# Kernel optimization log

Hardware: AMD Instinct MI355X
Metric: run time of the kernel (lower is better)

Reference implementation:

```python
import jax, jax.numpy as jnp
import numpy as np

N_NODES = 50000
N_EDGES = 800000
NEG_SLOPE = 0.2  # PyG GATConv default


def _glorot(key, shape):
    fan_in = shape[0] if len(shape) > 1 else shape[0]
    return jax.random.normal(key, shape, dtype=jnp.float32) / jnp.sqrt(jnp.float32(fan_in))


def setup_inputs() -> dict:
    key = jax.random.key(0)
    ks = jax.random.split(key, 12)
    x = jax.random.normal(ks[0], (N_NODES, 128), dtype=jnp.float32)
    edge_index = jax.random.randint(ks[1], (2, N_EDGES), 0, N_NODES, dtype=jnp.int64)
    return {
        "x": x,
        "edge_index": edge_index,
        # GAT layer 1: 128 -> 128 (heads=1)
        "W1": _glorot(ks[2], (128, 128)),
        "a_src1": _glorot(ks[3], (128,)),
        "a_dst1": _glorot(ks[4], (128,)),
        "b1": jnp.zeros((128,), dtype=jnp.float32),
        "Wres1": _glorot(ks[5], (128, 128)),
        # GAT layer 2: 128 -> 256
        "W2": _glorot(ks[6], (128, 256)),
        "a_src2": _glorot(ks[7], (256,)),
        "a_dst2": _glorot(ks[8], (256,)),
        "b2": jnp.zeros((256,), dtype=jnp.float32),
        "Wres2": _glorot(ks[9], (128, 256)),
    }


def _gat_layer(x, src, dst, W, a_src, a_dst, b, Wres, n):
    # h: [N, C_out] transformed node features
    h = x @ W
    # per-edge attention logit: gather scalar contributions, LeakyReLU
    logit = jax.nn.leaky_relu((h @ a_src)[src] + (h @ a_dst)[dst], NEG_SLOPE)  # [E]
    # numerically stable segment softmax over incoming edges of each dst node
    seg_max = jax.ops.segment_max(logit, dst, num_segments=n)  # [N]
    ex = jnp.exp(logit - seg_max[dst])
    denom = jax.ops.segment_sum(ex, dst, num_segments=n)  # [N]
    alpha = ex / denom[dst]  # [E]; self-loops guarantee denom > 0
    # weighted scatter-add aggregation
    out = jax.ops.segment_sum(alpha[:, None] * h[src], dst, num_segments=n)  # [N, C_out]
    # residual projection (in_dim != out_dim) + bias
    return out + x @ Wres + b


def reference(x, edge_index, W1, a_src1, a_dst1, b1, Wres1, W2, a_src2, a_dst2, b2, Wres2):
    n = x.shape[0]
    loops = jnp.arange(n, dtype=edge_index.dtype)  # add_self_loops=True (PyG default)
    src = jnp.concatenate([edge_index[0], loops])
    dst = jnp.concatenate([edge_index[1], loops])
    h = _gat_layer(x, src, dst, W1, a_src1, a_dst1, b1, Wres1, n)
    h = jax.nn.relu(h)
    return _gat_layer(h, src, dst, W2, a_src2, a_dst2, b2, Wres2, n)
```

## Files before the change

### kernel.cpp

```cpp
#include <hip/hip_runtime.h>
#include <math.h>

typedef __attribute__((ext_vector_type(8))) short bf16x8;
typedef __attribute__((ext_vector_type(4))) float f32x4;

__device__ inline unsigned short f2bf(float f) {
  union { float f; unsigned u; } x; x.f = f;
  unsigned r = x.u + 0x7FFF + ((x.u >> 16) & 1);
  return (unsigned short)(r >> 16);
}
__device__ inline float bf2f(unsigned short b) {
  union { unsigned u; float f; } x; x.u = ((unsigned)b) << 16;
  return x.f;
}


__global__ void convert_kernel(const void* edges, int E, int N,
                               int* __restrict__ src32, int* __restrict__ dst32,
                               int* __restrict__ counts) {
  int i = blockIdx.x * blockDim.x + threadIdx.x;
  int tot = E + N;
  if (i >= tot) return;
  int s, d;
  if (i < E) {
    const long long* q = (const long long*)edges;
    bool i64 = true;
#pragma unroll
    for (int k = 0; k < 8; ++k) {
      long long v = q[k];
      if (v < 0 || v >= (long long)N) i64 = false;
    }
    if (i64) {
      s = (int)q[i];
      d = (int)q[E + i];
    } else {
      s = ((const int*)edges)[i];
      d = ((const int*)edges)[E + i];
    }
  } else {
    s = d = i - E;
  }
  src32[i] = s;
  dst32[i] = d;
  atomicAdd(&counts[d], 1);
}


__global__ __launch_bounds__(256) void scan_partial(const int* __restrict__ counts,
                                                    int* __restrict__ bsum, int n) {
  int t = threadIdx.x;
  int base = blockIdx.x * 1024 + t * 4;
  int s = 0;
#pragma unroll
  for (int k = 0; k < 4; ++k) {
    int i = base + k;
    if (i < n) s += counts[i];
  }
#pragma unroll
  for (int off = 32; off; off >>= 1) s += __shfl_xor(s, off);
  __shared__ int red[4];
  if ((t & 63) == 0) red[t >> 6] = s;
  __syncthreads();
  if (t == 0) bsum[blockIdx.x] = red[0] + red[1] + red[2] + red[3];
}

__global__ __launch_bounds__(256) void scan_bsum(const int* __restrict__ bsum,
                                                 int* __restrict__ ebsum,
                                                 int* __restrict__ rowptr, int nblk, int n) {
  __shared__ int sh[256];
  int t = threadIdx.x;
  int v = (t < nblk) ? bsum[t] : 0;
  sh[t] = v;
  __syncthreads();
  for (int off = 1; off < 256; off <<= 1) {
    int u = (t >= off) ? sh[t - off] : 0;
    __syncthreads();
    sh[t] += u;
    __syncthreads();
  }
  if (t < nblk) ebsum[t] = sh[t] - v;
  if (t == nblk - 1) rowptr[n] = sh[t];
}

__global__ __launch_bounds__(256) void scan_final(const int* __restrict__ counts,
                                                  const int* __restrict__ ebsum,
                                                  int* __restrict__ rowptr,
                                                  int* __restrict__ cursor, int n) {
  int t = threadIdx.x;
  int lane = t & 63;
  int wv = t >> 6;
  int base = blockIdx.x * 1024 + t * 4;
  int c[4];
  int ts = 0;
#pragma unroll
  for (int k = 0; k < 4; ++k) {
    int i = base + k;
    c[k] = (i < n) ? counts[i] : 0;
    ts += c[k];
  }
  int ws = ts;
  for (int off = 1; off < 64; off <<= 1) {
    int u = __shfl_up(ws, off);
    if (lane >= off) ws += u;
  }
  __shared__ int wtot[4];
  if (lane == 63) wtot[wv] = ws;
  __syncthreads();
  int woff = 0;
  for (int k = 0; k < 4; ++k)
    if (k < wv) woff += wtot[k];
  int run = ebsum[blockIdx.x] + woff + (ws - ts);
#pragma unroll
  for (int k = 0; k < 4; ++k) {
    int i = base + k;
    if (i < n) {
      rowptr[i] = run;
      cursor[i] = run;
    }
    run += c[k];
  }
}

__global__ void scatter_kernel(const int* __restrict__ src32, const int* __restrict__ dst32,
                               int* __restrict__ cursor, int* __restrict__ csr_src, int tot) {
  int i = blockIdx.x * blockDim.x + threadIdx.x;
  if (i >= tot) return;
  int d = dst32[i];
  int slot = atomicAdd(&cursor[d], 1);
  csr_src[slot] = src32[i];
}


__global__ void cvt_x_kernel(const float* __restrict__ x, unsigned short* __restrict__ x16,
                             int N, int Mpad) {
  int tid = blockIdx.x * blockDim.x + threadIdx.x;
  if (tid >= Mpad * 32) return;
  int row = tid >> 5;
  int q = (tid & 31) << 2;
  unsigned short o0 = 0, o1 = 0, o2 = 0, o3 = 0;
  if (row < N) {
    float4 v = *(const float4*)(x + (size_t)row * 128 + q);
    o0 = f2bf(v.x); o1 = f2bf(v.y); o2 = f2bf(v.z); o3 = f2bf(v.w);
  }
  unsigned short* p = x16 + (size_t)row * 128 + q;
  p[0] = o0; p[1] = o1; p[2] = o2; p[3] = o3;
}

__global__ void cvt_wt_all(const float* __restrict__ W1, const float* __restrict__ Wres1,
                           const float* __restrict__ W2, const float* __restrict__ Wres2,
                           unsigned short* __restrict__ w1t, unsigned short* __restrict__ wres1t,
                           unsigned short* __restrict__ w2t, unsigned short* __restrict__ wres2t) {
  int tid = blockIdx.x * blockDim.x + threadIdx.x;
  const float* W;
  unsigned short* Wt;
  int C, loc;
  if (tid < 16384) { W = W1; Wt = w1t; C = 128; loc = tid; }
  else if (tid < 32768) { W = Wres1; Wt = wres1t; C = 128; loc = tid - 16384; }
  else if (tid < 65536) { W = W2; Wt = w2t; C = 256; loc = tid - 32768; }
  else if (tid < 98304) { W = Wres2; Wt = wres2t; C = 256; loc = tid - 65536; }
  else return;
  int c = loc >> 7;
  int k = loc & 127;
  Wt[(size_t)c * 128 + k] = f2bf(W[(size_t)k * C + c]);
}


template <int MODE>
__global__ __launch_bounds__(256) void gemm_mfma(const unsigned short* __restrict__ A,
                                                 const unsigned short* __restrict__ Bt,
                                                 void* __restrict__ Cout,
                                                 const float* __restrict__ bias,
                                                 int Nrows, int Ctot) {
  int l = threadIdx.x & 63;
  int w = threadIdx.x >> 6;
  int row_w = blockIdx.x * 128 + (w & 1) * 64;
  int col_w = blockIdx.y * 128 + (w >> 1) * 64;
  int lo = l & 15, hi = l >> 4;
  f32x4 acc[4][4];
#pragma unroll
  for (int i = 0; i < 4; ++i)
#pragma unroll
    for (int j = 0; j < 4; ++j) acc[i][j] = (f32x4){0.f, 0.f, 0.f, 0.f};

  const unsigned short* Ap = A + (size_t)(row_w + lo) * 128 + hi * 8;
  const unsigned short* Bp = Bt + (size_t)(col_w + lo) * 128 + hi * 8;
#pragma unroll
  for (int kk = 0; kk < 4; ++kk) {
    bf16x8 a[4], b[4];
#pragma unroll
    for (int f = 0; f < 4; ++f) {
      a[f] = *(const bf16x8*)(Ap + (size_t)f * 16 * 128 + kk * 32);
      b[f] = *(const bf16x8*)(Bp + (size_t)f * 16 * 128 + kk * 32);
    }
#pragma unroll
    for (int fr = 0; fr < 4; ++fr)
#pragma unroll
      for (int fc = 0; fc < 4; ++fc)
        acc[fr][fc] = __builtin_amdgcn_mfma_f32_16x16x32_bf16(a[fr], b[fc], acc[fr][fc], 0, 0, 0);
  }
#pragma unroll
  for (int fr = 0; fr < 4; ++fr) {
#pragma unroll
    for (int r = 0; r < 4; ++r) {
      int row = row_w + fr * 16 + hi * 4 + r;
      if (row < Nrows) {
#pragma unroll
        for (int fc = 0; fc < 4; ++fc) {
          int col = col_w + fc * 16 + lo;
          float v = acc[fr][fc][r];
          if (MODE != 0) v += bias[col];
          if (MODE == 2)
            ((float*)Cout)[(size_t)row * Ctot + col] = v;
          else
            ((unsigned short*)Cout)[(size_t)row * Ctot + col] = f2bf(v);
        }
      }
    }
  }
}


template <int C>
__global__ void scalars_kernel(const unsigned short* __restrict__ h,
                               const float* __restrict__ a_src,
                               const float* __restrict__ a_dst, float* __restrict__ as_,
                               float* __restrict__ ad_, int N) {
  int wid = (blockIdx.x * blockDim.x + threadIdx.x) >> 6;
  int lane = threadIdx.x & 63;
  if (wid >= N) return;
  const int FPL = C / 64;
  const unsigned short* hr = h + (size_t)wid * C + FPL * lane;
  float s1 = 0.f, s2 = 0.f;
#pragma unroll
  for (int j = 0; j < FPL; ++j) {
    float v = bf2f(hr[j]);
    s1 += v * a_src[FPL * lane + j];
    s2 += v * a_dst[FPL * lane + j];
  }
#pragma unroll
  for (int off = 32; off; off >>= 1) {
    s1 += __shfl_xor(s1, off);
    s2 += __shfl_xor(s2, off);
  }
  if (lane == 0) {
    as_[wid] = s1;
    ad_[wid] = s2;
  }
}


template <int C, bool BF16IO>
__global__ __launch_bounds__(256) void aggregate_kernel(
    const unsigned short* __restrict__ h, void* __restrict__ io,
    const float* __restrict__ as_, const float* __restrict__ ad_,
    const int* __restrict__ rowptr, const int* __restrict__ csr_src, int N) {
  const int FPL = C / 64;
  int wid = blockIdx.x * 4 + (threadIdx.x >> 6);
  int lane = threadIdx.x & 63;
  if (wid >= N) return;
  int base = rowptr[wid];
  int deg = rowptr[wid + 1] - base;
  float adn = ad_[wid];
  float m = -1e30f, ssum = 0.f;
  float acc[FPL];
#pragma unroll
  for (int c = 0; c < FPL; ++c) acc[c] = 0.f;
  for (int b0 = 0; b0 < deg; b0 += 64) {
    int idx = b0 + lane;
    int s = 0;
    float logit = -1e30f;
    if (idx < deg) {
      s = csr_src[base + idx];
      float tt = as_[s] + adn;
      logit = tt > 0.f ? tt : 0.2f * tt;
    }
    float cm = logit;
#pragma unroll
    for (int off = 32; off; off >>= 1) cm = fmaxf(cm, __shfl_xor(cm, off));
    float mnew = fmaxf(m, cm);
    float scale = __expf(m - mnew);
    ssum *= scale;
#pragma unroll
    for (int c = 0; c < FPL; ++c) acc[c] *= scale;
    float p = (idx < deg) ? __expf(logit - mnew) : 0.f;
    float ps = p;
#pragma unroll
    for (int off = 32; off; off >>= 1) ps += __shfl_xor(ps, off);
    ssum += ps;
    int cnt = min(64, deg - b0);
    for (int j = 0; j < cnt; ++j) {
      float pj = __shfl(p, j);
      int sj = __shfl(s, j);
      const unsigned short* hs = h + (size_t)sj * C + FPL * lane;
      if (FPL == 2) {
        ushort2 hv = *(const ushort2*)hs;
        acc[0] = fmaf(pj, bf2f(hv.x), acc[0]);
        acc[1] = fmaf(pj, bf2f(hv.y), acc[1]);
      } else {
        ushort4 hv = *(const ushort4*)hs;
        acc[0] = fmaf(pj, bf2f(hv.x), acc[0]);
        acc[1] = fmaf(pj, bf2f(hv.y), acc[1]);
        acc[2] = fmaf(pj, bf2f(hv.z), acc[2]);
        acc[3] = fmaf(pj, bf2f(hv.w), acc[3]);
      }
    }
    m = mnew;
  }
  float inv = 1.f / ssum;
  size_t o = (size_t)wid * C + FPL * lane;
  if (BF16IO) {
    unsigned short* p = (unsigned short*)io + o;
    ushort2 rv = *(const ushort2*)p;
    float v0 = fmaxf(acc[0] * inv + bf2f(rv.x), 0.f);
    float v1 = fmaxf(acc[1] * inv + bf2f(rv.y), 0.f);
    ushort2 ov; ov.x = f2bf(v0); ov.y = f2bf(v1);
    *(ushort2*)p = ov;
  } else {
    float* p = (float*)io + o;
    float4 rv = *(const float4*)p;
    float4 ov;
    ov.x = acc[0] * inv + rv.x;
    ov.y = acc[1] * inv + rv.y;
    ov.z = acc[2] * inv + rv.z;
    ov.w = acc[3] * inv + rv.w;
    *(float4*)p = ov;
  }
}


extern "C" void kernel_launch(void* const* d_in, const int* in_sizes, int n_in,
                              void* d_out, int out_size, void* d_ws, size_t ws_size,
                              hipStream_t stream) {
  const float* x = (const float*)d_in[0];
  const void* edges = d_in[1];
  const float* W1 = (const float*)d_in[2];
  const float* a_src1 = (const float*)d_in[3];
  const float* a_dst1 = (const float*)d_in[4];
  const float* b1 = (const float*)d_in[5];
  const float* Wres1 = (const float*)d_in[6];
  const float* W2 = (const float*)d_in[7];
  const float* a_src2 = (const float*)d_in[8];
  const float* a_dst2 = (const float*)d_in[9];
  const float* b2 = (const float*)d_in[10];
  const float* Wres2 = (const float*)d_in[11];
  float* out = (float*)d_out;

  int N = in_sizes[0] / 128;
  int E = in_sizes[1] / 2;
  int TOT = E + N;
  int Mpad = (N + 127) & ~127;
  int nblk = (N + 1023) >> 10;

  char* w = (char*)d_ws;
  size_t off = 0;
  auto alloc = [&](size_t bytes) {
    char* p = w + off;
    off += (bytes + 255) & ~(size_t)255;
    return p;
  };
  int* counts = (int*)alloc((size_t)N * 4);
  int* cursor = (int*)alloc((size_t)N * 4);
  int* rowptr = (int*)alloc((size_t)(N + 1) * 4);
  int* bsum = (int*)alloc(1024);
  int* ebsum = (int*)alloc(1024);
  float* as_ = (float*)alloc((size_t)N * 4);
  float* ad_ = (float*)alloc((size_t)N * 4);
  int* src32 = (int*)alloc((size_t)TOT * 4);
  int* dst32 = (int*)alloc((size_t)TOT * 4);
  int* csr = (int*)alloc((size_t)TOT * 4);
  unsigned short* x16 = (unsigned short*)alloc((size_t)Mpad * 128 * 2);
  unsigned short* w1t = (unsigned short*)alloc(128 * 128 * 2);
  unsigned short* wres1t = (unsigned short*)alloc(128 * 128 * 2);
  unsigned short* w2t = (unsigned short*)alloc(256 * 128 * 2);
  unsigned short* wres2t = (unsigned short*)alloc(256 * 128 * 2);
  unsigned short* h16 = (unsigned short*)alloc((size_t)N * 256 * 2);
  unsigned short* out1 = (unsigned short*)alloc((size_t)Mpad * 128 * 2);

  hipMemsetAsync(counts, 0, (size_t)N * 4, stream);
  hipMemsetAsync(out1 + (size_t)N * 128, 0, (size_t)(Mpad - N) * 128 * 2, stream);

  int gb = (TOT + 255) / 256;
  convert_kernel<<<gb, 256, 0, stream>>>(edges, E, N, src32, dst32, counts);
  scan_partial<<<nblk, 256, 0, stream>>>(counts, bsum, N);
  scan_bsum<<<1, 256, 0, stream>>>(bsum, ebsum, rowptr, nblk, N);
  scan_final<<<nblk, 256, 0, stream>>>(counts, ebsum, rowptr, cursor, N);
  scatter_kernel<<<gb, 256, 0, stream>>>(src32, dst32, cursor, csr, TOT);

  cvt_x_kernel<<<(Mpad * 32 + 255) / 256, 256, 0, stream>>>(x, x16, N, Mpad);
  cvt_wt_all<<<(98304 + 255) / 256, 256, 0, stream>>>(W1, Wres1, W2, Wres2, w1t, wres1t, w2t, wres2t);

  int mt = Mpad / 128;
  int sb = (N + 3) / 4;

  gemm_mfma<0><<<dim3(mt, 1), 256, 0, stream>>>(x16, w1t, h16, nullptr, N, 128);
  gemm_mfma<1><<<dim3(mt, 1), 256, 0, stream>>>(x16, wres1t, out1, b1, N, 128);
  scalars_kernel<128><<<sb, 256, 0, stream>>>(h16, a_src1, a_dst1, as_, ad_, N);
  aggregate_kernel<128, true><<<sb, 256, 0, stream>>>(h16, out1, as_, ad_, rowptr, csr, N);

  gemm_mfma<0><<<dim3(mt, 2), 256, 0, stream>>>(out1, w2t, h16, nullptr, N, 256);
  gemm_mfma<2><<<dim3(mt, 2), 256, 0, stream>>>(out1, wres2t, out, b2, N, 256);
  scalars_kernel<256><<<sb, 256, 0, stream>>>(h16, a_src2, a_dst2, as_, ad_, N);
  aggregate_kernel<256, false><<<sb, 256, 0, stream>>>(h16, out, as_, ad_, rowptr, csr, N);
}
```

Before: 429.8 us.

## Unroll aggregation gather by 4, store residual2 in bf16, merge conversion kernels

The edge-aggregation inner loop is unrolled four ways so four neighbour-row gathers are in flight at once, hiding more memory latency. The layer-2 residual projection now goes to a bf16 scratch buffer instead of read-modify-write on the fp32 output, which halves residual traffic. The x and weight conversion kernels are merged into one launch. The bf16 residual adds some rounding error to the final output.

```diff
diff --git a/kernel.cpp b/kernel.cpp
--- a/kernel.cpp
+++ b/kernel.cpp
@@ -131,33 +131,35 @@
 }
 
 
-__global__ void cvt_x_kernel(const float* __restrict__ x, unsigned short* __restrict__ x16,
-                             int N, int Mpad) {
+__global__ void cvt_all(const float* __restrict__ x,
+                        const float* __restrict__ W1, const float* __restrict__ Wres1,
+                        const float* __restrict__ W2, const float* __restrict__ Wres2,
+                        unsigned short* __restrict__ x16,
+                        unsigned short* __restrict__ w1t, unsigned short* __restrict__ wres1t,
+                        unsigned short* __restrict__ w2t, unsigned short* __restrict__ wres2t,
+                        int N, int Mpad) {
   int tid = blockIdx.x * blockDim.x + threadIdx.x;
-  if (tid >= Mpad * 32) return;
-  int row = tid >> 5;
-  int q = (tid & 31) << 2;
-  unsigned short o0 = 0, o1 = 0, o2 = 0, o3 = 0;
-  if (row < N) {
-    float4 v = *(const float4*)(x + (size_t)row * 128 + q);
-    o0 = f2bf(v.x); o1 = f2bf(v.y); o2 = f2bf(v.z); o3 = f2bf(v.w);
-  }
-  unsigned short* p = x16 + (size_t)row * 128 + q;
-  p[0] = o0; p[1] = o1; p[2] = o2; p[3] = o3;
-}
-
-__global__ void cvt_wt_all(const float* __restrict__ W1, const float* __restrict__ Wres1,
-                           const float* __restrict__ W2, const float* __restrict__ Wres2,
-                           unsigned short* __restrict__ w1t, unsigned short* __restrict__ wres1t,
-                           unsigned short* __restrict__ w2t, unsigned short* __restrict__ wres2t) {
-  int tid = blockIdx.x * blockDim.x + threadIdx.x;
+  int xcnt = Mpad * 32;
+  if (tid < xcnt) {
+    int row = tid >> 5;
+    int q = (tid & 31) << 2;
+    unsigned short o0 = 0, o1 = 0, o2 = 0, o3 = 0;
+    if (row < N) {
+      float4 v = *(const float4*)(x + (size_t)row * 128 + q);
+      o0 = f2bf(v.x); o1 = f2bf(v.y); o2 = f2bf(v.z); o3 = f2bf(v.w);
+    }
+    unsigned short* p = x16 + (size_t)row * 128 + q;
+    p[0] = o0; p[1] = o1; p[2] = o2; p[3] = o3;
+    return;
+  }
+  int t2 = tid - xcnt;
   const float* W;
   unsigned short* Wt;
   int C, loc;
-  if (tid < 16384) { W = W1; Wt = w1t; C = 128; loc = tid; }
-  else if (tid < 32768) { W = Wres1; Wt = wres1t; C = 128; loc = tid - 16384; }
-  else if (tid < 65536) { W = W2; Wt = w2t; C = 256; loc = tid - 32768; }
-  else if (tid < 98304) { W = Wres2; Wt = wres2t; C = 256; loc = tid - 65536; }
+  if (t2 < 16384) { W = W1; Wt = w1t; C = 128; loc = t2; }
+  else if (t2 < 32768) { W = Wres1; Wt = wres1t; C = 128; loc = t2 - 16384; }
+  else if (t2 < 65536) { W = W2; Wt = w2t; C = 256; loc = t2 - 32768; }
+  else if (t2 < 98304) { W = Wres2; Wt = wres2t; C = 256; loc = t2 - 65536; }
   else return;
   int c = loc >> 7;
   int k = loc & 127;
@@ -168,7 +170,7 @@
 template <int MODE>
 __global__ __launch_bounds__(256) void gemm_mfma(const unsigned short* __restrict__ A,
                                                  const unsigned short* __restrict__ Bt,
-                                                 void* __restrict__ Cout,
+                                                 unsigned short* __restrict__ Cout,
                                                  const float* __restrict__ bias,
                                                  int Nrows, int Ctot) {
   int l = threadIdx.x & 63;
@@ -208,11 +210,8 @@
         for (int fc = 0; fc < 4; ++fc) {
           int col = col_w + fc * 16 + lo;
           float v = acc[fr][fc][r];
-          if (MODE != 0) v += bias[col];
-          if (MODE == 2)
-            ((float*)Cout)[(size_t)row * Ctot + col] = v;
-          else
-            ((unsigned short*)Cout)[(size_t)row * Ctot + col] = f2bf(v);
+          if (MODE == 1) v += bias[col];
+          Cout[(size_t)row * Ctot + col] = f2bf(v);
         }
       }
     }
@@ -249,9 +248,10 @@
 }
 
 
-template <int C, bool BF16IO>
+template <int C, bool L1>
 __global__ __launch_bounds__(256) void aggregate_kernel(
-    const unsigned short* __restrict__ h, void* __restrict__ io,
+    const unsigned short* __restrict__ h, unsigned short* __restrict__ res,
+    float* __restrict__ outf,
     const float* __restrict__ as_, const float* __restrict__ ad_,
     const int* __restrict__ rowptr, const int* __restrict__ csr_src, int N) {
   const int FPL = C / 64;
@@ -288,7 +288,37 @@
     for (int off = 32; off; off >>= 1) ps += __shfl_xor(ps, off);
     ssum += ps;
     int cnt = min(64, deg - b0);
-    for (int j = 0; j < cnt; ++j) {
+    int j = 0;
+    for (; j + 4 <= cnt; j += 4) {
+      float pj0 = __shfl(p, j), pj1 = __shfl(p, j + 1);
+      float pj2 = __shfl(p, j + 2), pj3 = __shfl(p, j + 3);
+      int sj0 = __shfl(s, j), sj1 = __shfl(s, j + 1);
+      int sj2 = __shfl(s, j + 2), sj3 = __shfl(s, j + 3);
+      const unsigned short* h0 = h + (size_t)sj0 * C + FPL * lane;
+      const unsigned short* h1 = h + (size_t)sj1 * C + FPL * lane;
+      const unsigned short* h2 = h + (size_t)sj2 * C + FPL * lane;
+      const unsigned short* h3 = h + (size_t)sj3 * C + FPL * lane;
+      if (FPL == 2) {
+        ushort2 v0 = *(const ushort2*)h0, v1 = *(const ushort2*)h1;
+        ushort2 v2 = *(const ushort2*)h2, v3 = *(const ushort2*)h3;
+        acc[0] = fmaf(pj0, bf2f(v0.x), acc[0]); acc[1] = fmaf(pj0, bf2f(v0.y), acc[1]);
+        acc[0] = fmaf(pj1, bf2f(v1.x), acc[0]); acc[1] = fmaf(pj1, bf2f(v1.y), acc[1]);
+        acc[0] = fmaf(pj2, bf2f(v2.x), acc[0]); acc[1] = fmaf(pj2, bf2f(v2.y), acc[1]);
+        acc[0] = fmaf(pj3, bf2f(v3.x), acc[0]); acc[1] = fmaf(pj3, bf2f(v3.y), acc[1]);
+      } else {
+        ushort4 v0 = *(const ushort4*)h0, v1 = *(const ushort4*)h1;
+        ushort4 v2 = *(const ushort4*)h2, v3 = *(const ushort4*)h3;
+        acc[0] = fmaf(pj0, bf2f(v0.x), acc[0]); acc[1] = fmaf(pj0, bf2f(v0.y), acc[1]);
+        acc[2] = fmaf(pj0, bf2f(v0.z), acc[2]); acc[3] = fmaf(pj0, bf2f(v0.w), acc[3]);
+        acc[0] = fmaf(pj1, bf2f(v1.x), acc[0]); acc[1] = fmaf(pj1, bf2f(v1.y), acc[1]);
+        acc[2] = fmaf(pj1, bf2f(v1.z), acc[2]); acc[3] = fmaf(pj1, bf2f(v1.w), acc[3]);
+        acc[0] = fmaf(pj2, bf2f(v2.x), acc[0]); acc[1] = fmaf(pj2, bf2f(v2.y), acc[1]);
+        acc[2] = fmaf(pj2, bf2f(v2.z), acc[2]); acc[3] = fmaf(pj2, bf2f(v2.w), acc[3]);
+        acc[0] = fmaf(pj3, bf2f(v3.x), acc[0]); acc[1] = fmaf(pj3, bf2f(v3.y), acc[1]);
+        acc[2] = fmaf(pj3, bf2f(v3.z), acc[2]); acc[3] = fmaf(pj3, bf2f(v3.w), acc[3]);
+      }
+    }
+    for (; j < cnt; ++j) {
       float pj = __shfl(p, j);
       int sj = __shfl(s, j);
       const unsigned short* hs = h + (size_t)sj * C + FPL * lane;
@@ -308,22 +338,21 @@
   }
   float inv = 1.f / ssum;
   size_t o = (size_t)wid * C + FPL * lane;
-  if (BF16IO) {
-    unsigned short* p = (unsigned short*)io + o;
+  if (L1) {
+    unsigned short* p = res + o;
     ushort2 rv = *(const ushort2*)p;
     float v0 = fmaxf(acc[0] * inv + bf2f(rv.x), 0.f);
     float v1 = fmaxf(acc[1] * inv + bf2f(rv.y), 0.f);
     ushort2 ov; ov.x = f2bf(v0); ov.y = f2bf(v1);
     *(ushort2*)p = ov;
   } else {
-    float* p = (float*)io + o;
-    float4 rv = *(const float4*)p;
+    ushort4 rv = *(const ushort4*)(res + o);
     float4 ov;
-    ov.x = acc[0] * inv + rv.x;
-    ov.y = acc[1] * inv + rv.y;
-    ov.z = acc[2] * inv + rv.z;
-    ov.w = acc[3] * inv + rv.w;
-    *(float4*)p = ov;
+    ov.x = acc[0] * inv + bf2f(rv.x);
+    ov.y = acc[1] * inv + bf2f(rv.y);
+    ov.z = acc[2] * inv + bf2f(rv.z);
+    ov.w = acc[3] * inv + bf2f(rv.w);
+    *(float4*)(outf + o) = ov;
   }
 }
 
@@ -375,6 +404,7 @@
   unsigned short* wres2t = (unsigned short*)alloc(256 * 128 * 2);
   unsigned short* h16 = (unsigned short*)alloc((size_t)N * 256 * 2);
   unsigned short* out1 = (unsigned short*)alloc((size_t)Mpad * 128 * 2);
+  unsigned short* res2 = (unsigned short*)alloc((size_t)Mpad * 256 * 2);
 
   hipMemsetAsync(counts, 0, (size_t)N * 4, stream);
   hipMemsetAsync(out1 + (size_t)N * 128, 0, (size_t)(Mpad - N) * 128 * 2, stream);
@@ -386,8 +416,8 @@
   scan_final<<<nblk, 256, 0, stream>>>(counts, ebsum, rowptr, cursor, N);
   scatter_kernel<<<gb, 256, 0, stream>>>(src32, dst32, cursor, csr, TOT);
 
-  cvt_x_kernel<<<(Mpad * 32 + 255) / 256, 256, 0, stream>>>(x, x16, N, Mpad);
-  cvt_wt_all<<<(98304 + 255) / 256, 256, 0, stream>>>(W1, Wres1, W2, Wres2, w1t, wres1t, w2t, wres2t);
+  cvt_all<<<(Mpad * 32 + 98304 + 255) / 256, 256, 0, stream>>>(
+      x, W1, Wres1, W2, Wres2, x16, w1t, wres1t, w2t, wres2t, N, Mpad);
 
   int mt = Mpad / 128;
   int sb = (N + 3) / 4;
@@ -395,10 +425,10 @@
   gemm_mfma<0><<<dim3(mt, 1), 256, 0, stream>>>(x16, w1t, h16, nullptr, N, 128);
   gemm_mfma<1><<<dim3(mt, 1), 256, 0, stream>>>(x16, wres1t, out1, b1, N, 128);
   scalars_kernel<128><<<sb, 256, 0, stream>>>(h16, a_src1, a_dst1, as_, ad_, N);
-  aggregate_kernel<128, true><<<sb, 256, 0, stream>>>(h16, out1, as_, ad_, rowptr, csr, N);
+  aggregate_kernel<128, true><<<sb, 256, 0, stream>>>(h16, out1, nullptr, as_, ad_, rowptr, csr, N);
 
   gemm_mfma<0><<<dim3(mt, 2), 256, 0, stream>>>(out1, w2t, h16, nullptr, N, 256);
-  gemm_mfma<2><<<dim3(mt, 2), 256, 0, stream>>>(out1, wres2t, out, b2, N, 256);
+  gemm_mfma<1><<<dim3(mt, 2), 256, 0, stream>>>(out1, wres2t, res2, b2, N, 256);
   scalars_kernel<256><<<sb, 256, 0, stream>>>(h16, a_src2, a_dst2, as_, ad_, N);
-  aggregate_kernel<256, false><<<sb, 256, 0, stream>>>(h16, out, as_, ad_, rowptr, csr, N);
-}
+  aggregate_kernel<256, false><<<sb, 256, 0, stream>>>(h16, res2, out, as_, ad_, rowptr, csr, N);
+}
```

Measured after the change: 387.9 us. 1.11x faster.
